# Optimization experiments

Measured on AMD Instinct MI355X. Metric: run time of the kernel, lower is better.

## Reference

```python
import jax, jax.numpy as jnp
import numpy as np

B, S, K, N = 2, 2048, 4096, 16384

def setup_inputs() -> dict:
    key = jax.random.key(0)
    k1, k2, k3, k4 = jax.random.split(key, 4)
    x = jax.random.normal(k1, (B, S, K), dtype=jnp.float32)
    # int8-valued quantized weight stored as int32 for portability
    weight_q = jax.random.randint(k2, (N, K), -127, 128, dtype=jnp.int32)
    scale = jax.random.uniform(k3, (1,), dtype=jnp.float32, minval=0.01, maxval=0.05)
    bias = jax.random.normal(k4, (N,), dtype=jnp.float32)
    return {"x": x, "weight_q": weight_q, "scale": scale, "bias": bias}

def reference(x, weight_q, scale, bias):
    # Dequantize int8 weight with per-tensor symmetric scale, then column-parallel matmul.
    w = weight_q.astype(x.dtype) * scale  # [N, K]
    y = jnp.einsum('bsk,nk->bsn', x, w) + bias  # [B, S, N]
    return y
```

## Files before the change

### kernel.cpp

```cpp
#include <hip/hip_runtime.h>
#include <stdint.h>
#include <stddef.h>


#define M_TOT 4096
#define N_TOT 16384
#define K_TOT 4096
#define NT    64

typedef __attribute__((ext_vector_type(4))) int      v4i;
typedef __attribute__((ext_vector_type(8))) _Float16 f16x8;
typedef __attribute__((ext_vector_type(4))) float    f32x4;

#define GLOAD_LDS16(g, l) __builtin_amdgcn_global_load_lds(                  \
    (const __attribute__((address_space(1))) void*)(g),                      \
    (__attribute__((address_space(3))) void*)(l), 16, 0, 0)


__global__ __launch_bounds__(256) void cvt_x_i8(const float* __restrict__ x,
                                                signed char* __restrict__ o,
                                                float* __restrict__ sx) {
  const int row = blockIdx.x;
  const int tid = threadIdx.x;
  const float* xr = x + (size_t)row * K_TOT;
  float4 v[4];
  float mx = 0.f;
#pragma unroll
  for (int j = 0; j < 4; ++j) {
    v[j] = ((const float4*)xr)[tid * 4 + j];
    mx = fmaxf(mx, fmaxf(fmaxf(fabsf(v[j].x), fabsf(v[j].y)),
                         fmaxf(fabsf(v[j].z), fabsf(v[j].w))));
  }
#pragma unroll
  for (int off = 32; off; off >>= 1) mx = fmaxf(mx, __shfl_xor(mx, off));
  __shared__ float wm[4];
  if ((tid & 63) == 0) wm[tid >> 6] = mx;
  __syncthreads();
  const float m4 = fmaxf(fmaxf(wm[0], wm[1]), fmaxf(wm[2], wm[3]));
  const float smax = fmaxf(m4, 1e-6f);
  const float inv  = 127.0f / smax;
  if (tid == 0) sx[row] = smax / 127.0f;
  int p[4];
#pragma unroll
  for (int j = 0; j < 4; ++j) {
    int q0 = (int)rintf(v[j].x * inv), q1 = (int)rintf(v[j].y * inv);
    int q2 = (int)rintf(v[j].z * inv), q3 = (int)rintf(v[j].w * inv);
    q0 = max(-127, min(127, q0)); q1 = max(-127, min(127, q1));
    q2 = max(-127, min(127, q2)); q3 = max(-127, min(127, q3));
    p[j] = (q0 & 255) | ((q1 & 255) << 8) | ((q2 & 255) << 16) | (q3 << 24);
  }
  ((int4*)(o + (size_t)row * K_TOT))[tid] = make_int4(p[0], p[1], p[2], p[3]);
}

__global__ __launch_bounds__(256) void cvt_w_i8(const int* __restrict__ w,
                                                signed char* __restrict__ o, int n16) {
  const int stride = gridDim.x * blockDim.x;
  for (int i = blockIdx.x * blockDim.x + threadIdx.x; i < n16; i += stride) {
    int p[4];
#pragma unroll
    for (int j = 0; j < 4; ++j) {
      int4 a = ((const int4*)w)[i * 4 + j];
      p[j] = (a.x & 255) | ((a.y & 255) << 8) | ((a.z & 255) << 16) | (a.w << 24);
    }
    ((int4*)o)[i] = make_int4(p[0], p[1], p[2], p[3]);
  }
}


__device__ __forceinline__ void stage_i8(const signed char* __restrict__ g,
                                         size_t kbyte, signed char* l, int tid) {
#pragma unroll
  for (int j = 0; j < 2; ++j) {
    const int ci  = j * 512 + tid;
    const int row = ci >> 2;
    const int sc  = (ci & 3) ^ ((row >> 1) & 3);
    GLOAD_LDS16(g + (size_t)row * K_TOT + kbyte + sc * 16, l + ci * 16);
  }
}

__device__ __forceinline__ v4i fragi(const signed char* region, int r, int hi) {
  return *(const v4i*)(region + r * 64 + ((hi ^ ((r >> 1) & 3)) << 4));
}

#define BAR()    __builtin_amdgcn_s_barrier()

__global__ __launch_bounds__(512, 2) void gemm_i8(
    const signed char* __restrict__ A8, const signed char* __restrict__ B8,
    const float* __restrict__ sx, const float* __restrict__ scale_p,
    const float* __restrict__ bias, float* __restrict__ out)
{
  __shared__ __align__(16) signed char lds[3][2][16384];

  const int tid  = threadIdx.x;
  const int lane = tid & 63;
  const int wave = tid >> 6;
  const int wr = wave >> 2;
  const int wc = wave & 3;
  const int lr = lane & 15;
  const int hi = lane >> 4;

  const int bid = blockIdx.x;
  const int wg  = (bid & 7) * 128 + (bid >> 3);
  const int bm  = wg & 15;
  const int bn  = wg >> 4;
  const int arow0 = bm * 256;
  const int brow0 = bn * 256;

  const signed char* Ag = A8 + (size_t)arow0 * K_TOT;
  const signed char* Bg = B8 + (size_t)brow0 * K_TOT;

  v4i acc[8][4];
#pragma unroll
  for (int m = 0; m < 8; ++m)
#pragma unroll
    for (int n = 0; n < 4; ++n)
      acc[m][n] = (v4i){0, 0, 0, 0};

  stage_i8(Ag, 0,  &lds[0][0][0], tid);
  stage_i8(Bg, 0,  &lds[0][1][0], tid);
  stage_i8(Ag, 64, &lds[1][0][0], tid);
  stage_i8(Bg, 64, &lds[1][1][0], tid);
  asm volatile("s_waitcnt vmcnt(4)" ::: "memory");
  BAR();

  for (int t = 0; t < NT; ++t) {
    const signed char* At = &lds[t % 3][0][0];
    const signed char* Bt = &lds[t % 3][1][0];
    signed char* L2a = &lds[(t + 2) % 3][0][0];
    signed char* L2b = &lds[(t + 2) % 3][1][0];
    const size_t k2 = (size_t)(t + 2) * 64;

    if (t + 2 < NT) {
      stage_i8(Ag, k2, L2a, tid);
      stage_i8(Bg, k2, L2b, tid);
    }

    v4i af[8], bf[4];
#pragma unroll
    for (int m = 0; m < 8; ++m) af[m] = fragi(At, wr * 128 + m * 16 + lr, hi);
#pragma unroll
    for (int n = 0; n < 4; ++n) bf[n] = fragi(Bt, wc * 64 + n * 16 + lr, hi);
#pragma unroll
    for (int m = 0; m < 8; ++m)
#pragma unroll
      for (int n = 0; n < 4; ++n)
        acc[m][n] = __builtin_amdgcn_mfma_i32_16x16x64_i8(af[m], bf[n], acc[m][n], 0, 0, 0);

    if (t < NT - 2) asm volatile("s_waitcnt vmcnt(4)" ::: "memory");
    else            asm volatile("s_waitcnt vmcnt(0)" ::: "memory");
    BAR();
  }

  const float s = scale_p[0];
  float bv[4];
#pragma unroll
  for (int n = 0; n < 4; ++n) bv[n] = bias[brow0 + wc * 64 + n * 16 + lr];
#pragma unroll
  for (int mi = 0; mi < 8; ++mi) {
    const int row0 = arow0 + wr * 128 + (mi >> 2) * 64 + (mi & 3) * 16 + hi * 4;
    float sc4[4];
#pragma unroll
    for (int j = 0; j < 4; ++j) sc4[j] = sx[row0 + j] * s;
#pragma unroll
    for (int n = 0; n < 4; ++n) {
      const int col = brow0 + wc * 64 + n * 16 + lr;
      const v4i v = acc[mi][n];
#pragma unroll
      for (int j = 0; j < 4; ++j)
        out[(size_t)(row0 + j) * N_TOT + col] = (float)v[j] * sc4[j] + bv[n];
    }
  }
}


__global__ __launch_bounds__(256) void gemm_direct(
    const float* __restrict__ Xf, const int* __restrict__ Wq,
    const float* __restrict__ scale_p, const float* __restrict__ bias,
    float* __restrict__ out)
{
  __shared__ _Float16 ldsA[128 * 64];
  __shared__ _Float16 ldsB[128 * 64];
  const int tid = threadIdx.x, lane = tid & 63, wave = tid >> 6;
  const int wr = wave >> 1, wc = wave & 1;
  const int bid = blockIdx.x;
  const int wg  = (bid & 7) * 512 + (bid >> 3);
  const int arow0 = (wg & 31) * 128, brow0 = (wg >> 5) * 128;
  f32x4 acc[4][4];
#pragma unroll
  for (int m = 0; m < 4; ++m)
#pragma unroll
    for (int n = 0; n < 4; ++n) acc[m][n] = (f32x4){0.f, 0.f, 0.f, 0.f};
  const int srow = tid >> 3, schunk = tid & 7;
  const int lr = lane & 15, hi = lane >> 4;
  for (int kt = 0; kt < K_TOT / 64; ++kt) {
    const size_t kbase = (size_t)kt * 64;
    __syncthreads();
#pragma unroll
    for (int i = 0; i < 4; ++i) {
      const int row = i * 32 + srow;
      const int p = schunk ^ (row & 7);
      const float* gx = Xf + (size_t)(arow0 + row) * K_TOT + kbase + schunk * 8;
      const int*   gw = Wq + (size_t)(brow0 + row) * K_TOT + kbase + schunk * 8;
      float4 x0 = ((const float4*)gx)[0];
      float4 x1 = ((const float4*)gx)[1];
      int4   w0 = ((const int4*)gw)[0];
      int4   w1 = ((const int4*)gw)[1];
      f16x8 ha = { (_Float16)x0.x, (_Float16)x0.y, (_Float16)x0.z, (_Float16)x0.w,
                   (_Float16)x1.x, (_Float16)x1.y, (_Float16)x1.z, (_Float16)x1.w };
      f16x8 hb = { (_Float16)w0.x, (_Float16)w0.y, (_Float16)w0.z, (_Float16)w0.w,
                   (_Float16)w1.x, (_Float16)w1.y, (_Float16)w1.z, (_Float16)w1.w };
      *(f16x8*)(ldsA + row * 64 + p * 8) = ha;
      *(f16x8*)(ldsB + row * 64 + p * 8) = hb;
    }
    __syncthreads();
#pragma unroll
    for (int s2 = 0; s2 < 2; ++s2) {
      f16x8 af2[4], bf2[4];
#pragma unroll
      for (int m = 0; m < 4; ++m) {
        const int r = wr * 64 + m * 16 + lr;
        af2[m] = *(const f16x8*)(ldsA + r * 64 + (((s2 * 4 + hi) ^ (r & 7)) * 8));
      }
#pragma unroll
      for (int n = 0; n < 4; ++n) {
        const int r = wc * 64 + n * 16 + lr;
        bf2[n] = *(const f16x8*)(ldsB + r * 64 + (((s2 * 4 + hi) ^ (r & 7)) * 8));
      }
#pragma unroll
      for (int m = 0; m < 4; ++m)
#pragma unroll
        for (int n = 0; n < 4; ++n)
          acc[m][n] = __builtin_amdgcn_mfma_f32_16x16x32_f16(af2[m], bf2[n], acc[m][n], 0, 0, 0);
    }
  }
  const float s = scale_p[0];
#pragma unroll
  for (int n = 0; n < 4; ++n) {
    const int col = brow0 + wc * 64 + n * 16 + lr;
    const float bvv = bias[col];
#pragma unroll
    for (int m = 0; m < 4; ++m) {
      const int row0 = arow0 + wr * 64 + m * 16 + hi * 4;
      const f32x4 v = acc[m][n];
#pragma unroll
      for (int j = 0; j < 4; ++j)
        out[(size_t)(row0 + j) * N_TOT + col] = v[j] * s + bvv;
    }
  }
}


extern "C" void kernel_launch(void* const* d_in, const int* in_sizes, int n_in,
                              void* d_out, int out_size, void* d_ws, size_t ws_size,
                              hipStream_t stream) {
  const float* x     = (const float*)d_in[0];
  const int*   wq    = (const int*)d_in[1];
  const float* scale = (const float*)d_in[2];
  const float* bias  = (const float*)d_in[3];
  float*       out   = (float*)d_out;

  const size_t nA = (size_t)M_TOT * K_TOT;
  const size_t nB = (size_t)N_TOT * K_TOT;
  const size_t need = nA + nB + M_TOT * sizeof(float);

  if (ws_size >= need) {
    signed char* A8 = (signed char*)d_ws;
    signed char* B8 = A8 + nA;
    float*       sx = (float*)(B8 + nB);
    cvt_x_i8<<<M_TOT, 256, 0, stream>>>(x, A8, sx);
    cvt_w_i8<<<2048, 256, 0, stream>>>(wq, B8, (int)(nB / 16));
    gemm_i8<<<(M_TOT / 256) * (N_TOT / 256), 512, 0, stream>>>(A8, B8, sx, scale, bias, out);
  } else {
    gemm_direct<<<(M_TOT / 128) * (N_TOT / 128), 256, 0, stream>>>(x, wq, scale, bias, out);
  }
}
```

Before: 432.4 us.

## Deepen LDS ring to four stages and double-buffer MFMA fragments in registers

Grows the shared-memory ring from three to four K-tiles, so three tiles of global loads are in flight at once. The main loop is unrolled by two, and the next tile's LDS fragments are read into a second register set while MFMAs run on the current set. Adding sched_barrier after each s_barrier stops the compiler from moving instructions across the sync point. The cost is an extra 32 KB of LDS per block and about 48 more VGPRs for the second fragment set, which could cause spills under the 512x2 launch bounds.

```diff
diff --git a/kernel.cpp b/kernel.cpp
--- a/kernel.cpp
+++ b/kernel.cpp
@@ -82,14 +82,33 @@
   return *(const v4i*)(region + r * 64 + ((hi ^ ((r >> 1) & 3)) << 4));
 }
 
-#define BAR()    __builtin_amdgcn_s_barrier()
+#define BAR()  do { __builtin_amdgcn_s_barrier(); \
+                    __builtin_amdgcn_sched_barrier(0); } while (0)
+
+#define READ_FRAGS(A, B, At, Bt)                                              \
+  do {                                                                        \
+    _Pragma("unroll")                                                         \
+    for (int m = 0; m < 8; ++m) A[m] = fragi(At, wr * 128 + m * 16 + lr, hi); \
+    _Pragma("unroll")                                                         \
+    for (int n = 0; n < 4; ++n) B[n] = fragi(Bt, wc * 64 + n * 16 + lr, hi);  \
+  } while (0)
+
+#define MFMA_TILE(A, B)                                                       \
+  do {                                                                        \
+    _Pragma("unroll")                                                         \
+    for (int m = 0; m < 8; ++m)                                               \
+      _Pragma("unroll")                                                       \
+      for (int n = 0; n < 4; ++n)                                             \
+        acc[m][n] = __builtin_amdgcn_mfma_i32_16x16x64_i8(A[m], B[n],         \
+                                                          acc[m][n], 0, 0, 0);\
+  } while (0)
 
 __global__ __launch_bounds__(512, 2) void gemm_i8(
     const signed char* __restrict__ A8, const signed char* __restrict__ B8,
     const float* __restrict__ sx, const float* __restrict__ scale_p,
     const float* __restrict__ bias, float* __restrict__ out)
 {
-  __shared__ __align__(16) signed char lds[3][2][16384];
+  __shared__ __align__(16) signed char lds[4][2][16384];
 
   const int tid  = threadIdx.x;
   const int lane = tid & 63;
@@ -116,39 +135,49 @@
     for (int n = 0; n < 4; ++n)
       acc[m][n] = (v4i){0, 0, 0, 0};
 
-  stage_i8(Ag, 0,  &lds[0][0][0], tid);
-  stage_i8(Bg, 0,  &lds[0][1][0], tid);
-  stage_i8(Ag, 64, &lds[1][0][0], tid);
-  stage_i8(Bg, 64, &lds[1][1][0], tid);
+  stage_i8(Ag, 0,   &lds[0][0][0], tid);
+  stage_i8(Bg, 0,   &lds[0][1][0], tid);
+  stage_i8(Ag, 64,  &lds[1][0][0], tid);
+  stage_i8(Bg, 64,  &lds[1][1][0], tid);
+  stage_i8(Ag, 128, &lds[2][0][0], tid);
+  stage_i8(Bg, 128, &lds[2][1][0], tid);
   asm volatile("s_waitcnt vmcnt(4)" ::: "memory");
   BAR();
 
-  for (int t = 0; t < NT; ++t) {
-    const signed char* At = &lds[t % 3][0][0];
-    const signed char* Bt = &lds[t % 3][1][0];
-    signed char* L2a = &lds[(t + 2) % 3][0][0];
-    signed char* L2b = &lds[(t + 2) % 3][1][0];
-    const size_t k2 = (size_t)(t + 2) * 64;
-
-    if (t + 2 < NT) {
-      stage_i8(Ag, k2, L2a, tid);
-      stage_i8(Bg, k2, L2b, tid);
-    }
-
-    v4i af[8], bf[4];
-#pragma unroll
-    for (int m = 0; m < 8; ++m) af[m] = fragi(At, wr * 128 + m * 16 + lr, hi);
-#pragma unroll
-    for (int n = 0; n < 4; ++n) bf[n] = fragi(Bt, wc * 64 + n * 16 + lr, hi);
-#pragma unroll
-    for (int m = 0; m < 8; ++m)
-#pragma unroll
-      for (int n = 0; n < 4; ++n)
-        acc[m][n] = __builtin_amdgcn_mfma_i32_16x16x64_i8(af[m], bf[n], acc[m][n], 0, 0, 0);
-
-    if (t < NT - 2) asm volatile("s_waitcnt vmcnt(4)" ::: "memory");
-    else            asm volatile("s_waitcnt vmcnt(0)" ::: "memory");
-    BAR();
+  v4i a0[8], b0[4], a1[8], b1[4];
+  READ_FRAGS(a0, b0, &lds[0][0][0], &lds[0][1][0]);
+
+  for (int t = 0; t < NT; t += 2) {
+    {
+      if (t + 3 < NT) {
+        const size_t k3 = (size_t)(t + 3) * 64;
+        stage_i8(Ag, k3, &lds[(t + 3) & 3][0][0], tid);
+        stage_i8(Bg, k3, &lds[(t + 3) & 3][1][0], tid);
+      }
+      const signed char* At1 = &lds[(t + 1) & 3][0][0];
+      const signed char* Bt1 = &lds[(t + 1) & 3][1][0];
+      READ_FRAGS(a1, b1, At1, Bt1);
+      MFMA_TILE(a0, b0);
+      if (t + 3 < NT) asm volatile("s_waitcnt vmcnt(4)" ::: "memory");
+      else            asm volatile("s_waitcnt vmcnt(0)" ::: "memory");
+      BAR();
+    }
+    {
+      if (t + 4 < NT) {
+        const size_t k4 = (size_t)(t + 4) * 64;
+        stage_i8(Ag, k4, &lds[(t + 4) & 3][0][0], tid);
+        stage_i8(Bg, k4, &lds[(t + 4) & 3][1][0], tid);
+      }
+      if (t + 2 < NT) {
+        const signed char* At2 = &lds[(t + 2) & 3][0][0];
+        const signed char* Bt2 = &lds[(t + 2) & 3][1][0];
+        READ_FRAGS(a0, b0, At2, Bt2);
+      }
+      MFMA_TILE(a1, b1);
+      if (t + 4 < NT) asm volatile("s_waitcnt vmcnt(4)" ::: "memory");
+      else            asm volatile("s_waitcnt vmcnt(0)" ::: "memory");
+      BAR();
+    }
   }
 
   const float s = scale_p[0];
```

After: 417.4 us. 3.5% less time.

## Enlarge int8 GEMM block tile to 256x512 with 16 waves per block

Applied to the files above, without the earlier changes.

Doubles the N extent of the block tile and runs 1024 threads (16 waves) per block, reshaping the wave grid to 2x8 and splitting staging into separate A and B routines. Each wave keeps a 128x64 sub-tile. The goal is more reuse of each staged A tile, fewer blocks, and more resident waves per CU to hide latency, using about 144KB of LDS. The risk is register pressure: 1024-thread launch bounds leave about 128 registers per lane for a 128-register accumulator, which could cause spills.

```diff
diff --git a/kernel.cpp b/kernel.cpp
--- a/kernel.cpp
+++ b/kernel.cpp
@@ -7,6 +7,8 @@
 #define N_TOT 16384
 #define K_TOT 4096
 #define NT    64
+#define BM    256
+#define BN    512
 
 typedef __attribute__((ext_vector_type(4))) int      v4i;
 typedef __attribute__((ext_vector_type(8))) _Float16 f16x8;
@@ -67,11 +69,18 @@
 }
 
 
-__device__ __forceinline__ void stage_i8(const signed char* __restrict__ g,
-                                         size_t kbyte, signed char* l, int tid) {
+__device__ __forceinline__ void stage_A(const signed char* __restrict__ g,
+                                        size_t kbyte, signed char* l, int tid) {
+  const int row = tid >> 2;
+  const int sc  = (tid & 3) ^ ((row >> 1) & 3);
+  GLOAD_LDS16(g + (size_t)row * K_TOT + kbyte + sc * 16, l + tid * 16);
+}
+
+__device__ __forceinline__ void stage_B(const signed char* __restrict__ g,
+                                        size_t kbyte, signed char* l, int tid) {
 #pragma unroll
   for (int j = 0; j < 2; ++j) {
-    const int ci  = j * 512 + tid;
+    const int ci  = j * 1024 + tid;
     const int row = ci >> 2;
     const int sc  = (ci & 3) ^ ((row >> 1) & 3);
     GLOAD_LDS16(g + (size_t)row * K_TOT + kbyte + sc * 16, l + ci * 16);
@@ -84,27 +93,27 @@
 
 #define BAR()    __builtin_amdgcn_s_barrier()
 
-__global__ __launch_bounds__(512, 2) void gemm_i8(
+__global__ __launch_bounds__(1024) void gemm_i8(
     const signed char* __restrict__ A8, const signed char* __restrict__ B8,
     const float* __restrict__ sx, const float* __restrict__ scale_p,
     const float* __restrict__ bias, float* __restrict__ out)
 {
-  __shared__ __align__(16) signed char lds[3][2][16384];
+  __shared__ __align__(16) signed char lds[3][49152];
 
   const int tid  = threadIdx.x;
   const int lane = tid & 63;
   const int wave = tid >> 6;
-  const int wr = wave >> 2;
-  const int wc = wave & 3;
+  const int wr = wave >> 3;
+  const int wc = wave & 7;
   const int lr = lane & 15;
   const int hi = lane >> 4;
 
   const int bid = blockIdx.x;
-  const int wg  = (bid & 7) * 128 + (bid >> 3);
+  const int wg  = (bid & 7) * 64 + (bid >> 3);
   const int bm  = wg & 15;
   const int bn  = wg >> 4;
-  const int arow0 = bm * 256;
-  const int brow0 = bn * 256;
+  const int arow0 = bm * BM;
+  const int brow0 = bn * BN;
 
   const signed char* Ag = A8 + (size_t)arow0 * K_TOT;
   const signed char* Bg = B8 + (size_t)brow0 * K_TOT;
@@ -116,23 +125,22 @@
     for (int n = 0; n < 4; ++n)
       acc[m][n] = (v4i){0, 0, 0, 0};
 
-  stage_i8(Ag, 0,  &lds[0][0][0], tid);
-  stage_i8(Bg, 0,  &lds[0][1][0], tid);
-  stage_i8(Ag, 64, &lds[1][0][0], tid);
-  stage_i8(Bg, 64, &lds[1][1][0], tid);
-  asm volatile("s_waitcnt vmcnt(4)" ::: "memory");
+  stage_A(Ag, 0,  &lds[0][0],     tid);
+  stage_B(Bg, 0,  &lds[0][16384], tid);
+  stage_A(Ag, 64, &lds[1][0],     tid);
+  stage_B(Bg, 64, &lds[1][16384], tid);
+  asm volatile("s_waitcnt vmcnt(3)" ::: "memory");
   BAR();
 
   for (int t = 0; t < NT; ++t) {
-    const signed char* At = &lds[t % 3][0][0];
-    const signed char* Bt = &lds[t % 3][1][0];
-    signed char* L2a = &lds[(t + 2) % 3][0][0];
-    signed char* L2b = &lds[(t + 2) % 3][1][0];
-    const size_t k2 = (size_t)(t + 2) * 64;
+    const signed char* At = &lds[t % 3][0];
+    const signed char* Bt = &lds[t % 3][16384];
 
     if (t + 2 < NT) {
-      stage_i8(Ag, k2, L2a, tid);
-      stage_i8(Bg, k2, L2b, tid);
+      const size_t k2 = (size_t)(t + 2) * 64;
+      signed char* L2 = &lds[(t + 2) % 3][0];
+      stage_A(Ag, k2, L2, tid);
+      stage_B(Bg, k2, L2 + 16384, tid);
     }
 
     v4i af[8], bf[4];
@@ -146,7 +154,7 @@
       for (int n = 0; n < 4; ++n)
         acc[m][n] = __builtin_amdgcn_mfma_i32_16x16x64_i8(af[m], bf[n], acc[m][n], 0, 0, 0);
 
-    if (t < NT - 2) asm volatile("s_waitcnt vmcnt(4)" ::: "memory");
+    if (t < NT - 2) asm volatile("s_waitcnt vmcnt(3)" ::: "memory");
     else            asm volatile("s_waitcnt vmcnt(0)" ::: "memory");
     BAR();
   }
@@ -269,7 +277,7 @@
     float*       sx = (float*)(B8 + nB);
     cvt_x_i8<<<M_TOT, 256, 0, stream>>>(x, A8, sx);
     cvt_w_i8<<<2048, 256, 0, stream>>>(wq, B8, (int)(nB / 16));
-    gemm_i8<<<(M_TOT / 256) * (N_TOT / 256), 512, 0, stream>>>(A8, B8, sx, scale, bias, out);
+    gemm_i8<<<(M_TOT / BM) * (N_TOT / BN), 1024, 0, stream>>>(A8, B8, sx, scale, bias, out);
   } else {
     gemm_direct<<<(M_TOT / 128) * (N_TOT / 128), 256, 0, stream>>>(x, wq, scale, bias, out);
   }
```

New measurement: 1.657 ms. +283.3%, slower.

## Double the K tile to 128 bytes and switch to double-buffered LDS

Applied to the files above, without the earlier changes.

Each main-loop iteration now stages a 128-byte K slice per row instead of 64, with an 8-way XOR swizzle to match. The triple-buffered prefetch two tiles ahead becomes a double buffer that prefetches one tile ahead, and the K loop runs half as many iterations. This halves the number of barriers and waitcnt points per block and gives each iteration twice as many MFMAs between syncs. In exchange the prefetch distance is shorter and the kernel now waits for all loads (vmcnt(0)) every iteration, which can expose memory latency. LDS use grows from 96KB to 128KB per block.

```diff
diff --git a/kernel.cpp b/kernel.cpp
--- a/kernel.cpp
+++ b/kernel.cpp
@@ -6,7 +6,7 @@
 #define M_TOT 4096
 #define N_TOT 16384
 #define K_TOT 4096
-#define NT    64
+#define NT    32
 
 typedef __attribute__((ext_vector_type(4))) int      v4i;
 typedef __attribute__((ext_vector_type(8))) _Float16 f16x8;
@@ -67,19 +67,19 @@
 }
 
 
-__device__ __forceinline__ void stage_i8(const signed char* __restrict__ g,
+__device__ __forceinline__ void stage128(const signed char* __restrict__ g,
                                          size_t kbyte, signed char* l, int tid) {
 #pragma unroll
-  for (int j = 0; j < 2; ++j) {
+  for (int j = 0; j < 4; ++j) {
     const int ci  = j * 512 + tid;
-    const int row = ci >> 2;
-    const int sc  = (ci & 3) ^ ((row >> 1) & 3);
+    const int row = ci >> 3;
+    const int sc  = (ci & 7) ^ (row & 7);
     GLOAD_LDS16(g + (size_t)row * K_TOT + kbyte + sc * 16, l + ci * 16);
   }
 }
 
-__device__ __forceinline__ v4i fragi(const signed char* region, int r, int hi) {
-  return *(const v4i*)(region + r * 64 + ((hi ^ ((r >> 1) & 3)) << 4));
+__device__ __forceinline__ v4i frag128(const signed char* region, int r, int ch) {
+  return *(const v4i*)(region + r * 128 + ((ch ^ (r & 7)) << 4));
 }
 
 #define BAR()    __builtin_amdgcn_s_barrier()
@@ -89,7 +89,7 @@
     const float* __restrict__ sx, const float* __restrict__ scale_p,
     const float* __restrict__ bias, float* __restrict__ out)
 {
-  __shared__ __align__(16) signed char lds[3][2][16384];
+  __shared__ __align__(16) signed char lds[2][2][32768];
 
   const int tid  = threadIdx.x;
   const int lane = tid & 63;
@@ -116,38 +116,39 @@
     for (int n = 0; n < 4; ++n)
       acc[m][n] = (v4i){0, 0, 0, 0};
 
-  stage_i8(Ag, 0,  &lds[0][0][0], tid);
-  stage_i8(Bg, 0,  &lds[0][1][0], tid);
-  stage_i8(Ag, 64, &lds[1][0][0], tid);
-  stage_i8(Bg, 64, &lds[1][1][0], tid);
-  asm volatile("s_waitcnt vmcnt(4)" ::: "memory");
+  stage128(Ag, 0, &lds[0][0][0], tid);
+  stage128(Bg, 0, &lds[0][1][0], tid);
+  asm volatile("s_waitcnt vmcnt(0)" ::: "memory");
   BAR();
 
   for (int t = 0; t < NT; ++t) {
-    const signed char* At = &lds[t % 3][0][0];
-    const signed char* Bt = &lds[t % 3][1][0];
-    signed char* L2a = &lds[(t + 2) % 3][0][0];
-    signed char* L2b = &lds[(t + 2) % 3][1][0];
-    const size_t k2 = (size_t)(t + 2) * 64;
-
-    if (t + 2 < NT) {
-      stage_i8(Ag, k2, L2a, tid);
-      stage_i8(Bg, k2, L2b, tid);
-    }
-
-    v4i af[8], bf[4];
-#pragma unroll
-    for (int m = 0; m < 8; ++m) af[m] = fragi(At, wr * 128 + m * 16 + lr, hi);
-#pragma unroll
-    for (int n = 0; n < 4; ++n) bf[n] = fragi(Bt, wc * 64 + n * 16 + lr, hi);
-#pragma unroll
-    for (int m = 0; m < 8; ++m)
+    const int b = t & 1;
+    const signed char* At = &lds[b][0][0];
+    const signed char* Bt = &lds[b][1][0];
+
+    if (t + 1 < NT) {
+      const size_t k1 = (size_t)(t + 1) * 128;
+      stage128(Ag, k1, &lds[b ^ 1][0][0], tid);
+      stage128(Bg, k1, &lds[b ^ 1][1][0], tid);
+    }
+
+#pragma unroll
+    for (int kk = 0; kk < 2; ++kk) {
+      v4i af[8], bf[4];
+#pragma unroll
+      for (int m = 0; m < 8; ++m)
+        af[m] = frag128(At, wr * 128 + m * 16 + lr, kk * 4 + hi);
 #pragma unroll
       for (int n = 0; n < 4; ++n)
-        acc[m][n] = __builtin_amdgcn_mfma_i32_16x16x64_i8(af[m], bf[n], acc[m][n], 0, 0, 0);
-
-    if (t < NT - 2) asm volatile("s_waitcnt vmcnt(4)" ::: "memory");
-    else            asm volatile("s_waitcnt vmcnt(0)" ::: "memory");
+        bf[n] = frag128(Bt, wc * 64 + n * 16 + lr, kk * 4 + hi);
+#pragma unroll
+      for (int m = 0; m < 8; ++m)
+#pragma unroll
+        for (int n = 0; n < 4; ++n)
+          acc[m][n] = __builtin_amdgcn_mfma_i32_16x16x64_i8(af[m], bf[n], acc[m][n], 0, 0, 0);
+    }
+
+    asm volatile("s_waitcnt vmcnt(0)" ::: "memory");
     BAR();
   }
 
```

Result: faster. 410.7 us (-5.0%).
